# Performance work log

Measured on AMD Instinct MI355X. Metric: run time of the kernel, lower is better.

## Reference

```python
import jax, jax.numpy as jnp
import numpy as np

SQRT2 = 1.4142135623730951
MH_C = 0.8673250705840776  # (2/sqrt(3)) * pi**(-1/4), mexican-hat normalizer


def _bn(x, eps=1e-5):
    # BatchNorm (training-mode batch stats, default affine gamma=1, beta=0)
    mu = jnp.mean(x, axis=0, keepdims=True)
    var = jnp.var(x, axis=0, keepdims=True)
    return (x - mu) / jnp.sqrt(var + eps)


def setup_inputs() -> dict:
    key = jax.random.key(0)
    ks = jax.random.split(key, 10)
    N, F, E, B, OUT = 1024, 1024, 32768, 16, 10
    H = F // 2  # 512 after Haar DWT
    x = jax.random.normal(ks[0], (N, F), dtype=jnp.float32)
    edge_index = jax.random.randint(ks[1], (2, E), 0, N, dtype=jnp.int32)
    batch = jnp.sort(jax.random.randint(ks[2], (N,), 0, B, dtype=jnp.int32))
    w_att = jax.random.normal(ks[3], (2,), dtype=jnp.float32)  # Linear(2,1,bias=False)
    wk_scale = jnp.ones((H, H), dtype=jnp.float32)
    wk_trans = jax.random.normal(ks[4], (H, H), dtype=jnp.float32) * 0.1
    wk_wav_w = jax.random.normal(ks[5], (H, H), dtype=jnp.float32) * 0.05
    wk_base_w = jax.random.normal(ks[6], (H, H), dtype=jnp.float32) * 0.05
    fc1_w = jax.random.normal(ks[7], (512, F + H), dtype=jnp.float32) * 0.02
    fc1_b = jnp.zeros((512,), dtype=jnp.float32)
    fc2_w = jax.random.normal(ks[8], (OUT, 512), dtype=jnp.float32) * 0.02
    fc2_b = jnp.zeros((OUT,), dtype=jnp.float32)
    return {"x": x, "w_att": w_att, "wk_scale": wk_scale, "wk_trans": wk_trans,
            "wk_wav_w": wk_wav_w, "wk_base_w": wk_base_w, "fc1_w": fc1_w,
            "fc1_b": fc1_b, "fc2_w": fc2_w, "fc2_b": fc2_b,
            "edge_index": edge_index, "batch": batch, "num_graphs": B}


def reference(x, w_att, wk_scale, wk_trans, wk_wav_w, wk_base_w,
              fc1_w, fc1_b, fc2_w, fc2_b, edge_index, batch, num_graphs):
    N = x.shape[0]
    # --- WaveletAttention: Haar ('db1') DWT over the feature dim ---
    xe, xo = x[:, 0::2], x[:, 1::2]
    low = (xe + xo) / SQRT2            # [N, 512]
    high = (xe - xo) / SQRT2           # [N, 512]
    scores = jax.nn.sigmoid(low * w_att[0] + high * w_att[1])
    h = scores * low + (1.0 - scores) * high
    # --- GINConv aggregation (eps=0): self + sum of neighbor features ---
    src, dst = edge_index[0], edge_index[1]
    agg = h + jax.ops.segment_sum(h[src], dst, num_segments=N)  # [N, 512]
    # --- WavKAN layer 512->512 (mexican hat) ---
    xs = (agg[:, None, :] - wk_trans) / wk_scale                # [N, 512, 512]
    xs2 = xs * xs
    mh = MH_C * (1.0 - xs2) * jnp.exp(-0.5 * xs2)
    wav = jnp.einsum('noi,oi->no', mh, wk_wav_w)                # [N, 512]
    base = jax.nn.silu(agg) @ wk_base_w.T
    conv_out = _bn(wav + base)   # WavKAN-internal BatchNorm1d
    conv_out = _bn(conv_out)     # bn1 (dropout p=0 -> identity)
    # --- skip concat + bn2 ---
    z = _bn(jnp.concatenate([x, conv_out], axis=1))             # [N, 1536]
    # --- global mean pool over graphs ---
    sums = jax.ops.segment_sum(z, batch, num_segments=num_graphs)
    cnts = jax.ops.segment_sum(jnp.ones((N,), z.dtype), batch, num_segments=num_graphs)
    pooled = sums / jnp.maximum(cnts, 1.0)[:, None]             # [B, 1536]
    # --- classifier head (eval-mode dropout = identity) ---
    h1 = jax.nn.relu(pooled @ fc1_w.T + fc1_b)
    return h1 @ fc2_w.T + fc2_b
```

## Files before the change

### kernel.cpp

```cpp
#include <hip/hip_runtime.h>
#include <math.h>

#define N_NODES 1024
#define F_DIM   1024
#define H_DIM   512
#define E_EDGES 32768
#define B_GRAPHS 16
#define OUT_DIM 10
#define FH_DIM  1536
#define EPS 1e-5f
#define MH_C_D 0.8673250705840776
#define C2_D   0.72134752044448170368
#define C2_F   ((float)C2_D)
#define CSC    0.84932180028801904272f
#define WC2F   ((float)(MH_C_D / C2_D))
#define INV_SQRT2 0.70710678118654752440f

typedef float v2f __attribute__((ext_vector_type(2)));
typedef unsigned int u32;
typedef const __attribute__((address_space(1))) u32 gu32;
typedef __attribute__((address_space(3))) u32 lu32;

#if __has_builtin(__builtin_amdgcn_exp2f)
#define EXP2NEG(x) __builtin_amdgcn_exp2f(-(x))
#else
#define EXP2NEG(x) __expf(-0.69314718055994530942f * (x))
#endif

#define PK_FMA_BB(d, a, p) \
    asm("v_pk_fma_f32 %0, %1, %2, %2 op_sel:[0,0,1] op_sel_hi:[1,0,1]" \
        : "=v"(d) : "v"(a), "v"(p))
#define PK_MUL2(d, a, b) \
    asm("v_pk_mul_f32 %0, %1, %2" : "=v"(d) : "v"(a), "v"(b))
#define PK_WZC(d, s, k) \
    asm("v_pk_mul_f32 %0, %1, %2 op_sel:[0,0] op_sel_hi:[0,1]" \
        : "=v"(d) : "v"(s), "v"(k))
#define PK_FMA_HI_ACC(acc, s, p) \
    asm("v_pk_fma_f32 %0, %1, %2, %0 op_sel:[0,1,0] op_sel_hi:[1,1,1]" \
        : "+v"(acc) : "v"(s), "v"(p))

__global__ __launch_bounds__(256) void k_setup(const float* __restrict__ x,
                                               const float* __restrict__ watt,
                                               float* __restrict__ h,
                                               float* __restrict__ zbase) {
    const int bid = blockIdx.x;
    const int t = threadIdx.x;
    if (bid < 2048) {
        int idx = bid * 256 + t;
        float2 p = ((const float2*)x)[idx];
        float lo = (p.x + p.y) * INV_SQRT2;
        float hi = (p.x - p.y) * INV_SQRT2;
        float tt = lo * watt[0] + hi * watt[1];
        float sc = 1.0f / (1.0f + __expf(-tt));
        h[idx] = sc * lo + (1.0f - sc) * hi;
    } else {
        zbase[(bid - 2048) * 256 + t] = 0.0f;
    }
}

__global__ __launch_bounds__(256) void k_hx(const int* __restrict__ dst,
                                            int* __restrict__ deg,
                                            const float* __restrict__ x,
                                            float* __restrict__ xsum,
                                            float* __restrict__ xsum2,
                                            const float* __restrict__ scale,
                                            const float* __restrict__ trans,
                                            const float* __restrict__ ww,
                                            const float* __restrict__ bw,
                                            float* __restrict__ pk) {
    const int bid = blockIdx.x;
    const int t = threadIdx.x;
    if (bid < 128) {
        int e = bid * 256 + t;
        atomicAdd(&deg[dst[e]], 1);
    } else if (bid < 192) {
        const int n0 = (bid - 128) * 16;
        float s[4] = {}, s2[4] = {};
        for (int r = 0; r < 16; ++r) {
            #pragma unroll
            for (int ch = 0; ch < 4; ++ch) {
                float v = x[(n0 + r) * F_DIM + ch * 256 + t];
                s[ch] += v; s2[ch] += v * v;
            }
        }
        #pragma unroll
        for (int ch = 0; ch < 4; ++ch) {
            unsafeAtomicAdd(&xsum[ch * 256 + t], s[ch]);
            unsafeAtomicAdd(&xsum2[ch * 256 + t], s2[ch]);
        }
    } else {
        int g = (bid - 192) * 256 + t;
        float iv = 1.0f / scale[g];
        float4 p;
        p.x = iv * CSC;
        p.y = -(trans[g] * iv * CSC);
        p.z = -(ww[g] * WC2F);
        p.w = bw[g];
        ((float4*)pk)[g] = p;
    }
}

__global__ __launch_bounds__(1024) void k_scan(const int* __restrict__ deg,
                                               int* __restrict__ start,
                                               int* __restrict__ cursor) {
    __shared__ int wsum[16];
    int t = threadIdx.x;
    int lane = t & 63, wid = t >> 6;
    int v = deg[t];
    int x = v;
    #pragma unroll
    for (int off = 1; off < 64; off <<= 1) {
        int y = __shfl_up(x, off, 64);
        if (lane >= off) x += y;
    }
    if (lane == 63) wsum[wid] = x;
    __syncthreads();
    if (t < 16) {
        int w = wsum[t];
        int xs = w;
        #pragma unroll
        for (int off = 1; off < 16; off <<= 1) {
            int y = __shfl_up(xs, off, 64);
            if (t >= off) xs += y;
        }
        wsum[t] = xs - w;
    }
    __syncthreads();
    int excl = wsum[wid] + x - v;
    start[t] = excl;
    cursor[t] = excl;
}

__global__ __launch_bounds__(256) void k_fill(const int* __restrict__ src,
                                              const int* __restrict__ dst,
                                              int* __restrict__ cursor,
                                              int* __restrict__ elist) {
    int e = blockIdx.x * 256 + threadIdx.x;
    int slot = atomicAdd(&cursor[dst[e]], 1);
    elist[slot] = src[e];
}

__global__ __launch_bounds__(256) void k_gather(const float* __restrict__ h,
                                                const int* __restrict__ start,
                                                const int* __restrict__ deg,
                                                const int* __restrict__ elist,
                                                float* __restrict__ agg) {
    int d = blockIdx.x;
    int t = threadIdx.x;
    int st = start[d], dg = deg[d];
    const float2* h2 = (const float2*)h;
    float2 a = h2[d * 256 + t];
    int k = 0;
    for (; k + 4 <= dg; k += 4) {
        int s0 = elist[st + k];
        int s1 = elist[st + k + 1];
        int s2 = elist[st + k + 2];
        int s3 = elist[st + k + 3];
        float2 v0 = h2[s0 * 256 + t];
        float2 v1 = h2[s1 * 256 + t];
        float2 v2 = h2[s2 * 256 + t];
        float2 v3 = h2[s3 * 256 + t];
        a.x += (v0.x + v1.x) + (v2.x + v3.x);
        a.y += (v0.y + v1.y) + (v2.y + v3.y);
    }
    for (; k < dg; ++k) {
        int s0 = elist[st + k];
        float2 v0 = h2[s0 * 256 + t];
        a.x += v0.x; a.y += v0.y;
    }
    ((float2*)agg)[d * 256 + t] = a;
}

__global__ __launch_bounds__(256) void k_transpose(const float* __restrict__ agg,
                                                   float* __restrict__ aggT,
                                                   float* __restrict__ siluT) {
    __shared__ float tile[64 * 65];
    const int t = threadIdx.x;
    const int n0 = blockIdx.x * 64;
    const int i0 = blockIdx.y * 64;
    #pragma unroll
    for (int v = 0; v < 4; ++v) {
        int flat = v * 256 + t;
        int r = flat >> 4, c4 = flat & 15;
        float4 a = *(const float4*)&agg[(n0 + r) * H_DIM + i0 + c4 * 4];
        tile[(c4 * 4 + 0) * 65 + r] = a.x;
        tile[(c4 * 4 + 1) * 65 + r] = a.y;
        tile[(c4 * 4 + 2) * 65 + r] = a.z;
        tile[(c4 * 4 + 3) * 65 + r] = a.w;
    }
    __syncthreads();
    #pragma unroll
    for (int v = 0; v < 4; ++v) {
        int flat = v * 256 + t;
        int il = flat >> 4, c4 = flat & 15;
        float4 a;
        a.x = tile[il * 65 + c4 * 4 + 0];
        a.y = tile[il * 65 + c4 * 4 + 1];
        a.z = tile[il * 65 + c4 * 4 + 2];
        a.w = tile[il * 65 + c4 * 4 + 3];
        int g = (i0 + il) * N_NODES + n0 + c4 * 4;
        *(float4*)&aggT[g] = a;
        float4 s;
        s.x = a.x / (1.0f + __expf(-a.x));
        s.y = a.y / (1.0f + __expf(-a.y));
        s.z = a.z / (1.0f + __expf(-a.z));
        s.w = a.w / (1.0f + __expf(-a.w));
        *(float4*)&siluT[g] = s;
    }
}

#define TN 128
#define TO 32
#define KI 16
#define TOP (TO + 1)
#define ZSPLIT 8
#define ZLEN (H_DIM / ZSPLIT)
#define NSTG (ZLEN / KI)
__global__ __launch_bounds__(256) void k_wavelet(const float* __restrict__ aggT,
                                                 const float* __restrict__ siluT,
                                                 const float* __restrict__ pk,
                                                 float* __restrict__ vbp) {
    __shared__ float  sA[2][KI * TN];
    __shared__ float  sS[2][KI * TN];
    __shared__ float4 sP4[2][KI * TOP];

    const int t  = threadIdx.x;
    const int n0 = blockIdx.x * TN;
    const int o0 = blockIdx.y * TO;
    const int z0 = blockIdx.z * ZLEN;
    const int na = (t & 15) * 4;
    const int ol = (t >> 4) * 2;

    const int srow = t >> 5, scol = (t & 31) * 4;
    const int po  = t >> 4;
    const int pii = t & 15;
    const float4* pk4 = (const float4*)pk;

    v2f accw[2][4] = {};
    v2f accb[2][4] = {};
    v2f kC2; kC2.x = 1.0f; kC2.y = -C2_F;

    {
        int g0 = (z0 + srow) * N_NODES + n0 + scol;
        int g1 = (z0 + 8 + srow) * N_NODES + n0 + scol;
        __builtin_amdgcn_global_load_lds((gu32*)&aggT[g0],  (lu32*)&sA[0][t * 4], 16, 0, 0);
        __builtin_amdgcn_global_load_lds((gu32*)&aggT[g1],  (lu32*)&sA[0][1024 + t * 4], 16, 0, 0);
        __builtin_amdgcn_global_load_lds((gu32*)&siluT[g0], (lu32*)&sS[0][t * 4], 16, 0, 0);
        __builtin_amdgcn_global_load_lds((gu32*)&siluT[g1], (lu32*)&sS[0][1024 + t * 4], 16, 0, 0);
        float4 r0 = pk4[(size_t)(o0 + po) * H_DIM + z0 + pii];
        float4 r1 = pk4[(size_t)(o0 + po + 16) * H_DIM + z0 + pii];
        sP4[0][pii * TOP + po]      = r0;
        sP4[0][pii * TOP + po + 16] = r1;
    }
    __syncthreads();

    for (int stg = 0; stg < NSTG; ++stg) {
        const int i0 = z0 + stg * KI;
        const int nb = (stg + 1) & 1;
        float4 r0, r1;
        if (stg + 1 < NSTG) {
            int g0 = (i0 + KI + srow) * N_NODES + n0 + scol;
            int g1 = (i0 + KI + 8 + srow) * N_NODES + n0 + scol;
            __builtin_amdgcn_global_load_lds((gu32*)&aggT[g0],
                                             (lu32*)&sA[nb][t * 4], 16, 0, 0);
            __builtin_amdgcn_global_load_lds((gu32*)&aggT[g1],
                                             (lu32*)&sA[nb][1024 + t * 4], 16, 0, 0);
            __builtin_amdgcn_global_load_lds((gu32*)&siluT[g0],
                                             (lu32*)&sS[nb][t * 4], 16, 0, 0);
            __builtin_amdgcn_global_load_lds((gu32*)&siluT[g1],
                                             (lu32*)&sS[nb][1024 + t * 4], 16, 0, 0);
            r0 = pk4[(size_t)(o0 + po) * H_DIM + i0 + KI + pii];
            r1 = pk4[(size_t)(o0 + po + 16) * H_DIM + i0 + KI + pii];
        }
        const float*  pA = sA[stg & 1];
        const float*  pS = sS[stg & 1];
        const float4* pP = sP4[stg & 1];
        #pragma unroll 4
        for (int ii = 0; ii < KI; ++ii) {
            float4 af0 = *(const float4*)&pA[ii * TN + na];
            float4 af1 = *(const float4*)&pA[ii * TN + 64 + na];
            float4 sf0 = *(const float4*)&pS[ii * TN + na];
            float4 sf1 = *(const float4*)&pS[ii * TN + 64 + na];
            v2f a01 = {af0.x, af0.y}, a23 = {af0.z, af0.w};
            v2f a45 = {af1.x, af1.y}, a67 = {af1.z, af1.w};
            v2f s01 = {sf0.x, sf0.y}, s23 = {sf0.z, sf0.w};
            v2f s45 = {sf1.x, sf1.y}, s67 = {sf1.z, sf1.w};
            #pragma unroll
            for (int oo = 0; oo < 2; ++oo) {
                float4 pq = pP[ii * TOP + ol + oo];
                v2f pxy = {pq.x, pq.y};
                v2f pzw = {pq.z, pq.w};
                v2f wzc; PK_WZC(wzc, pzw, kC2);
                v2f y0, y1, y2, y3, q0, q1, q2, q3, w0, w1, w2, w3;
                PK_FMA_BB(y0, a01, pxy); PK_FMA_BB(y1, a23, pxy);
                PK_FMA_BB(y2, a45, pxy); PK_FMA_BB(y3, a67, pxy);
                PK_MUL2(q0, y0, y0); PK_MUL2(q1, y1, y1);
                PK_MUL2(q2, y2, y2); PK_MUL2(q3, y3, y3);
                PK_FMA_BB(w0, q0, wzc); PK_FMA_BB(w1, q1, wzc);
                PK_FMA_BB(w2, q2, wzc); PK_FMA_BB(w3, q3, wzc);
                accw[oo][0].x += w0.x * EXP2NEG(q0.x);
                accw[oo][0].y += w0.y * EXP2NEG(q0.y);
                accw[oo][1].x += w1.x * EXP2NEG(q1.x);
                accw[oo][1].y += w1.y * EXP2NEG(q1.y);
                accw[oo][2].x += w2.x * EXP2NEG(q2.x);
                accw[oo][2].y += w2.y * EXP2NEG(q2.y);
                accw[oo][3].x += w3.x * EXP2NEG(q3.x);
                accw[oo][3].y += w3.y * EXP2NEG(q3.y);
                PK_FMA_HI_ACC(accb[oo][0], s01, pzw);
                PK_FMA_HI_ACC(accb[oo][1], s23, pzw);
                PK_FMA_HI_ACC(accb[oo][2], s45, pzw);
                PK_FMA_HI_ACC(accb[oo][3], s67, pzw);
            }
        }
        if (stg + 1 < NSTG) {
            sP4[nb][pii * TOP + po]      = r0;
            sP4[nb][pii * TOP + po + 16] = r1;
        }
        __syncthreads();
    }
    float* out = vbp + (size_t)blockIdx.z * (N_NODES * H_DIM);
    #pragma unroll
    for (int p = 0; p < 4; ++p) {
        int rn = n0 + ((p & 2) ? 64 : 0) + na + (p & 1) * 2;
        float2 lo, hi;
        lo.x = accw[0][p].x + accb[0][p].x;
        lo.y = accw[1][p].x + accb[1][p].x;
        hi.x = accw[0][p].y + accb[0][p].y;
        hi.y = accw[1][p].y + accb[1][p].y;
        *(float2*)&out[(size_t)rn * H_DIM + o0 + ol]       = lo;
        *(float2*)&out[(size_t)(rn + 1) * H_DIM + o0 + ol] = hi;
    }
}

__global__ __launch_bounds__(256) void k_reduce(const float* __restrict__ vbp,
                                                float* __restrict__ vb,
                                                float* __restrict__ colsum,
                                                float* __restrict__ colsum2) {
    const int b = blockIdx.x;
    const int o0 = (b & 7) * 64;
    const int n0 = (b >> 3) * 64;
    const int t = threadIdx.x;
    const int oc = o0 + (t & 63);
    const int nsub = t >> 6;
    float s = 0.f, s2 = 0.f;
    for (int r = 0; r < 16; ++r) {
        int n = n0 + r * 4 + nsub;
        size_t idx = (size_t)n * H_DIM + oc;
        float v = 0.f;
        #pragma unroll
        for (int z = 0; z < ZSPLIT; ++z) v += vbp[z * (N_NODES * H_DIM) + idx];
        vb[idx] = v;
        s += v; s2 += v * v;
    }
    __shared__ float sh1[256], sh2[256];
    sh1[t] = s; sh2[t] = s2;
    __syncthreads();
    if (t < 64) {
        s  = sh1[t] + sh1[t + 64] + sh1[t + 128] + sh1[t + 192];
        s2 = sh2[t] + sh2[t + 64] + sh2[t + 128] + sh2[t + 192];
        unsafeAtomicAdd(&colsum[o0 + t], s);
        unsafeAtomicAdd(&colsum2[o0 + t], s2);
    }
}

__global__ __launch_bounds__(256) void k_pool(const float* __restrict__ x,
                                              const float* __restrict__ vb,
                                              const int* __restrict__ batch,
                                              const float* __restrict__ colsum,
                                              const float* __restrict__ colsum2,
                                              const float* __restrict__ xsum,
                                              const float* __restrict__ xsum2,
                                              float* __restrict__ pooled) {
    const int b = blockIdx.x;
    const int ch = blockIdx.y;
    const int t = threadIdx.x;

    __shared__ int s_cnt[4];
    __shared__ int s_st;
    int c = 0;
    for (int n = t; n < N_NODES; n += 256) {
        int bb = batch[n];
        int pb = (n == 0) ? -1 : batch[n - 1];
        c += (bb == b) ? 1 : 0;
        if (bb == b && pb != b) s_st = n;
    }
    #pragma unroll
    for (int off = 32; off > 0; off >>= 1) c += __shfl_down(c, off);
    if ((t & 63) == 0) s_cnt[t >> 6] = c;
    __syncthreads();
    int cnt = s_cnt[0] + s_cnt[1] + s_cnt[2] + s_cnt[3];
    int st = (cnt > 0) ? s_st : 0;
    float ic = (cnt > 0) ? 1.0f / (float)cnt : 0.f;

    float acc = 0.f;
    if (ch < 4) {
        int col = ch * 256 + t;
        float mu  = xsum[col] * (1.0f / N_NODES);
        float var = xsum2[col] * (1.0f / N_NODES) - mu * mu;
        if (var < 0.f) var = 0.f;
        float S = 1.0f / sqrtf(var + EPS);
        const float* base = x + col;
        for (int r = 0; r < cnt; ++r) acc += base[(size_t)(st + r) * F_DIM];
        pooled[b * FH_DIM + col] = (acc * ic - mu) * S;
    } else {
        int col = (ch - 4) * 256 + t;
        float mu  = colsum[col] * (1.0f / N_NODES);
        float var = colsum2[col] * (1.0f / N_NODES) - mu * mu;
        if (var < 0.f) var = 0.f;
        float s1v = 1.0f / sqrtf(var + EPS);
        float v1  = var * s1v * s1v;
        float s2v = 1.0f / sqrtf(v1 + EPS);
        float v2  = v1 * s2v * s2v;
        float s3v = 1.0f / sqrtf(v2 + EPS);
        float S = s1v * s2v * s3v;
        const float* base = vb + col;
        for (int r = 0; r < cnt; ++r) acc += base[(size_t)(st + r) * H_DIM];
        pooled[b * FH_DIM + F_DIM + col] = (acc * ic - mu) * S;
    }
}

__global__ __launch_bounds__(256) void k_fc1(const float* __restrict__ pooled,
                                             const float* __restrict__ w,
                                             const float* __restrict__ bias,
                                             float* __restrict__ h1) {
    int wid = (blockIdx.x * 256 + threadIdx.x) >> 6;
    int lane = threadIdx.x & 63;
    int b = wid >> 9, o = wid & 511;
    const float4* pr = (const float4*)(pooled + b * FH_DIM);
    const float4* wr = (const float4*)(w + o * FH_DIM);
    float acc = 0.f;
    #pragma unroll
    for (int k = 0; k < 6; ++k) {
        float4 a = pr[k * 64 + lane];
        float4 v = wr[k * 64 + lane];
        acc += a.x * v.x + a.y * v.y + a.z * v.z + a.w * v.w;
    }
    #pragma unroll
    for (int off = 32; off > 0; off >>= 1) acc += __shfl_down(acc, off);
    if (lane == 0) h1[b * H_DIM + o] = fmaxf(acc + bias[o], 0.f);
}

__global__ __launch_bounds__(256) void k_fc2(const float* __restrict__ h1,
                                             const float* __restrict__ w,
                                             const float* __restrict__ bias,
                                             float* __restrict__ outp) {
    int wid = (blockIdx.x * 256 + threadIdx.x) >> 6;
    int lane = threadIdx.x & 63;
    if (wid >= B_GRAPHS * OUT_DIM) return;
    int b = wid / OUT_DIM, u = wid % OUT_DIM;
    const float4* hr = (const float4*)(h1 + b * H_DIM);
    const float4* wr = (const float4*)(w + u * H_DIM);
    float acc = 0.f;
    #pragma unroll
    for (int k = 0; k < 2; ++k) {
        float4 a = hr[k * 64 + lane];
        float4 v = wr[k * 64 + lane];
        acc += a.x * v.x + a.y * v.y + a.z * v.z + a.w * v.w;
    }
    #pragma unroll
    for (int off = 32; off > 0; off >>= 1) acc += __shfl_down(acc, off);
    if (lane == 0) outp[b * OUT_DIM + u] = acc + bias[u];
}

extern "C" void kernel_launch(void* const* d_in, const int* in_sizes, int n_in,
                              void* d_out, int out_size, void* d_ws, size_t ws_size,
                              hipStream_t stream) {
    const float* x       = (const float*)d_in[0];
    const float* w_att   = (const float*)d_in[1];
    const float* wk_scale= (const float*)d_in[2];
    const float* wk_trans= (const float*)d_in[3];
    const float* wk_wav  = (const float*)d_in[4];
    const float* wk_base = (const float*)d_in[5];
    const float* fc1_w   = (const float*)d_in[6];
    const float* fc1_b   = (const float*)d_in[7];
    const float* fc2_w   = (const float*)d_in[8];
    const float* fc2_b   = (const float*)d_in[9];
    const int*   eidx    = (const int*)d_in[10];
    const int*   batch   = (const int*)d_in[11];
    float* outp = (float*)d_out;

    float* ws = (float*)d_ws;
    const int NH = N_NODES * H_DIM;
    float* h      = ws;
    float* agg    = h + NH;
    float* aggT   = agg + NH;
    float* siluT  = aggT + NH;
    float* pk     = siluT + NH;
    float* vbp    = pk + 4 * (H_DIM * H_DIM);
    float* vb     = vbp + (size_t)ZSPLIT * NH;
    float* colsum = vb + NH;
    float* colsum2= colsum + 512;
    float* xsum   = colsum2 + 512;
    float* xsum2  = xsum + 1024;
    int*   deg    = (int*)(xsum2 + 1024);
    int*   estart = deg + N_NODES;
    int*   cursor = estart + N_NODES;
    int*   elist  = cursor + N_NODES;
    float* pooled = (float*)(elist + E_EDGES);
    float* h1     = pooled + B_GRAPHS * FH_DIM;

    const int* src = eidx;
    const int* dst = eidx + E_EDGES;

    k_setup<<<2064, 256, 0, stream>>>(x, w_att, h, colsum);
    k_hx<<<1216, 256, 0, stream>>>(dst, deg, x, xsum, xsum2,
                                   wk_scale, wk_trans, wk_wav, wk_base, pk);
    k_scan<<<1, N_NODES, 0, stream>>>(deg, estart, cursor);
    k_fill<<<E_EDGES / 256, 256, 0, stream>>>(src, dst, cursor, elist);
    k_gather<<<N_NODES, 256, 0, stream>>>(h, estart, deg, elist, agg);
    {
        dim3 grid(N_NODES / 64, H_DIM / 64);
        k_transpose<<<grid, 256, 0, stream>>>(agg, aggT, siluT);
    }
    {
        dim3 grid(N_NODES / TN, H_DIM / TO, ZSPLIT);
        k_wavelet<<<grid, 256, 0, stream>>>(aggT, siluT, pk, vbp);
    }
    k_reduce<<<128, 256, 0, stream>>>(vbp, vb, colsum, colsum2);
    {
        dim3 grid(B_GRAPHS, 6);
        k_pool<<<grid, 256, 0, stream>>>(x, vb, batch, colsum, colsum2, xsum, xsum2, pooled);
    }
    k_fc1<<<(B_GRAPHS * H_DIM * 64) / 256, 256, 0, stream>>>(pooled, fc1_w, fc1_b, h1);
    k_fc2<<<(B_GRAPHS * OUT_DIM * 64 + 255) / 256, 256, 0, stream>>>(h1, fc2_w, fc2_b, outp);
}
```

Baseline: 197.6 us.

## Merge setup into k_hx and fuse pool, fc1, fc2 into one head kernel

Folds the Haar/attention setup work into the existing multi-role k_hx launch and replaces the zeroing blocks with a hipMemsetAsync covering the colsum/xsum accumulators. It also fuses mean pooling, fc1 and fc2 into a single k_head kernel with one 1024-thread block per graph, keeping pooled and h1 in shared memory. The aim is to remove several launch gaps and global round-trips of intermediate buffers. The cost is that the head now runs on only 16 blocks, and each block rereads the whole fc1 weight matrix with far less parallelism.

```diff
diff --git a/kernel.cpp b/kernel.cpp
--- a/kernel.cpp
+++ b/kernel.cpp
@@ -39,10 +39,18 @@
     asm("v_pk_fma_f32 %0, %1, %2, %0 op_sel:[0,1,0] op_sel_hi:[1,1,1]" \
         : "+v"(acc) : "v"(s), "v"(p))
 
-__global__ __launch_bounds__(256) void k_setup(const float* __restrict__ x,
-                                               const float* __restrict__ watt,
-                                               float* __restrict__ h,
-                                               float* __restrict__ zbase) {
+__global__ __launch_bounds__(256) void k_hx(const int* __restrict__ dst,
+                                            int* __restrict__ deg,
+                                            const float* __restrict__ x,
+                                            float* __restrict__ xsum,
+                                            float* __restrict__ xsum2,
+                                            const float* __restrict__ scale,
+                                            const float* __restrict__ trans,
+                                            const float* __restrict__ ww,
+                                            const float* __restrict__ bw,
+                                            float* __restrict__ pk,
+                                            const float* __restrict__ watt,
+                                            float* __restrict__ h) {
     const int bid = blockIdx.x;
     const int t = threadIdx.x;
     if (bid < 2048) {
@@ -53,28 +61,20 @@
         float tt = lo * watt[0] + hi * watt[1];
         float sc = 1.0f / (1.0f + __expf(-tt));
         h[idx] = sc * lo + (1.0f - sc) * hi;
+    } else if (bid < 3072) {
+        int g = (bid - 2048) * 256 + t;
+        float iv = 1.0f / scale[g];
+        float4 p;
+        p.x = iv * CSC;
+        p.y = -(trans[g] * iv * CSC);
+        p.z = -(ww[g] * WC2F);
+        p.w = bw[g];
+        ((float4*)pk)[g] = p;
+    } else if (bid < 3200) {
+        int e = (bid - 3072) * 256 + t;
+        atomicAdd(&deg[dst[e]], 1);
     } else {
-        zbase[(bid - 2048) * 256 + t] = 0.0f;
-    }
-}
-
-__global__ __launch_bounds__(256) void k_hx(const int* __restrict__ dst,
-                                            int* __restrict__ deg,
-                                            const float* __restrict__ x,
-                                            float* __restrict__ xsum,
-                                            float* __restrict__ xsum2,
-                                            const float* __restrict__ scale,
-                                            const float* __restrict__ trans,
-                                            const float* __restrict__ ww,
-                                            const float* __restrict__ bw,
-                                            float* __restrict__ pk) {
-    const int bid = blockIdx.x;
-    const int t = threadIdx.x;
-    if (bid < 128) {
-        int e = bid * 256 + t;
-        atomicAdd(&deg[dst[e]], 1);
-    } else if (bid < 192) {
-        const int n0 = (bid - 128) * 16;
+        const int n0 = (bid - 3200) * 16;
         float s[4] = {}, s2[4] = {};
         for (int r = 0; r < 16; ++r) {
             #pragma unroll
@@ -88,15 +88,6 @@
             unsafeAtomicAdd(&xsum[ch * 256 + t], s[ch]);
             unsafeAtomicAdd(&xsum2[ch * 256 + t], s2[ch]);
         }
-    } else {
-        int g = (bid - 192) * 256 + t;
-        float iv = 1.0f / scale[g];
-        float4 p;
-        p.x = iv * CSC;
-        p.y = -(trans[g] * iv * CSC);
-        p.z = -(ww[g] * WC2F);
-        p.w = bw[g];
-        ((float4*)pk)[g] = p;
     }
 }
 
@@ -363,47 +354,55 @@
     }
 }
 
-__global__ __launch_bounds__(256) void k_pool(const float* __restrict__ x,
-                                              const float* __restrict__ vb,
-                                              const int* __restrict__ batch,
-                                              const float* __restrict__ colsum,
-                                              const float* __restrict__ colsum2,
-                                              const float* __restrict__ xsum,
-                                              const float* __restrict__ xsum2,
-                                              float* __restrict__ pooled) {
+__global__ __launch_bounds__(1024) void k_head(const float* __restrict__ x,
+                                               const float* __restrict__ vb,
+                                               const int* __restrict__ batch,
+                                               const float* __restrict__ colsum,
+                                               const float* __restrict__ colsum2,
+                                               const float* __restrict__ xsum,
+                                               const float* __restrict__ xsum2,
+                                               const float* __restrict__ fc1w,
+                                               const float* __restrict__ fc1b,
+                                               const float* __restrict__ fc2w,
+                                               const float* __restrict__ fc2b,
+                                               float* __restrict__ outp) {
+    __shared__ __align__(16) float sp[FH_DIM];
+    __shared__ __align__(16) float sh1v[H_DIM];
+    __shared__ int s_cnt[16];
+    __shared__ int s_st;
     const int b = blockIdx.x;
-    const int ch = blockIdx.y;
     const int t = threadIdx.x;
-
-    __shared__ int s_cnt[4];
-    __shared__ int s_st;
-    int c = 0;
-    for (int n = t; n < N_NODES; n += 256) {
-        int bb = batch[n];
-        int pb = (n == 0) ? -1 : batch[n - 1];
-        c += (bb == b) ? 1 : 0;
-        if (bb == b && pb != b) s_st = n;
-    }
+    const int lane = t & 63, wv = t >> 6;
+
+    {
+        int bb = batch[t];
+        int pb = (t == 0) ? -1 : batch[t - 1];
+        int c = (bb == b) ? 1 : 0;
+        if (bb == b && pb != b) s_st = t;
+        #pragma unroll
+        for (int off = 32; off > 0; off >>= 1) c += __shfl_down(c, off);
+        if (lane == 0) s_cnt[wv] = c;
+    }
+    __syncthreads();
+    int cnt = 0;
     #pragma unroll
-    for (int off = 32; off > 0; off >>= 1) c += __shfl_down(c, off);
-    if ((t & 63) == 0) s_cnt[t >> 6] = c;
-    __syncthreads();
-    int cnt = s_cnt[0] + s_cnt[1] + s_cnt[2] + s_cnt[3];
+    for (int q = 0; q < 16; ++q) cnt += s_cnt[q];
     int st = (cnt > 0) ? s_st : 0;
     float ic = (cnt > 0) ? 1.0f / (float)cnt : 0.f;
 
-    float acc = 0.f;
-    if (ch < 4) {
-        int col = ch * 256 + t;
+    {
+        int col = t;
         float mu  = xsum[col] * (1.0f / N_NODES);
         float var = xsum2[col] * (1.0f / N_NODES) - mu * mu;
         if (var < 0.f) var = 0.f;
         float S = 1.0f / sqrtf(var + EPS);
+        float acc = 0.f;
         const float* base = x + col;
         for (int r = 0; r < cnt; ++r) acc += base[(size_t)(st + r) * F_DIM];
-        pooled[b * FH_DIM + col] = (acc * ic - mu) * S;
-    } else {
-        int col = (ch - 4) * 256 + t;
+        sp[col] = (acc * ic - mu) * S;
+    }
+    if (t < H_DIM) {
+        int col = t;
         float mu  = colsum[col] * (1.0f / N_NODES);
         float var = colsum2[col] * (1.0f / N_NODES) - mu * mu;
         if (var < 0.f) var = 0.f;
@@ -413,53 +412,46 @@
         float v2  = v1 * s2v * s2v;
         float s3v = 1.0f / sqrtf(v2 + EPS);
         float S = s1v * s2v * s3v;
+        float acc = 0.f;
         const float* base = vb + col;
         for (int r = 0; r < cnt; ++r) acc += base[(size_t)(st + r) * H_DIM];
-        pooled[b * FH_DIM + F_DIM + col] = (acc * ic - mu) * S;
-    }
-}
-
-__global__ __launch_bounds__(256) void k_fc1(const float* __restrict__ pooled,
-                                             const float* __restrict__ w,
-                                             const float* __restrict__ bias,
-                                             float* __restrict__ h1) {
-    int wid = (blockIdx.x * 256 + threadIdx.x) >> 6;
-    int lane = threadIdx.x & 63;
-    int b = wid >> 9, o = wid & 511;
-    const float4* pr = (const float4*)(pooled + b * FH_DIM);
-    const float4* wr = (const float4*)(w + o * FH_DIM);
-    float acc = 0.f;
-    #pragma unroll
-    for (int k = 0; k < 6; ++k) {
-        float4 a = pr[k * 64 + lane];
-        float4 v = wr[k * 64 + lane];
-        acc += a.x * v.x + a.y * v.y + a.z * v.z + a.w * v.w;
-    }
-    #pragma unroll
-    for (int off = 32; off > 0; off >>= 1) acc += __shfl_down(acc, off);
-    if (lane == 0) h1[b * H_DIM + o] = fmaxf(acc + bias[o], 0.f);
-}
-
-__global__ __launch_bounds__(256) void k_fc2(const float* __restrict__ h1,
-                                             const float* __restrict__ w,
-                                             const float* __restrict__ bias,
-                                             float* __restrict__ outp) {
-    int wid = (blockIdx.x * 256 + threadIdx.x) >> 6;
-    int lane = threadIdx.x & 63;
-    if (wid >= B_GRAPHS * OUT_DIM) return;
-    int b = wid / OUT_DIM, u = wid % OUT_DIM;
-    const float4* hr = (const float4*)(h1 + b * H_DIM);
-    const float4* wr = (const float4*)(w + u * H_DIM);
-    float acc = 0.f;
-    #pragma unroll
-    for (int k = 0; k < 2; ++k) {
-        float4 a = hr[k * 64 + lane];
-        float4 v = wr[k * 64 + lane];
-        acc += a.x * v.x + a.y * v.y + a.z * v.z + a.w * v.w;
-    }
-    #pragma unroll
-    for (int off = 32; off > 0; off >>= 1) acc += __shfl_down(acc, off);
-    if (lane == 0) outp[b * OUT_DIM + u] = acc + bias[u];
+        sp[F_DIM + col] = (acc * ic - mu) * S;
+    }
+    __syncthreads();
+
+    {
+        const float4* pr = (const float4*)sp;
+        for (int oi = 0; oi < 32; ++oi) {
+            int o = wv * 32 + oi;
+            const float4* wr = (const float4*)(fc1w + o * FH_DIM);
+            float acc = 0.f;
+            #pragma unroll
+            for (int k = 0; k < 6; ++k) {
+                float4 aa = pr[k * 64 + lane];
+                float4 vv = wr[k * 64 + lane];
+                acc += aa.x * vv.x + aa.y * vv.y + aa.z * vv.z + aa.w * vv.w;
+            }
+            #pragma unroll
+            for (int off = 32; off > 0; off >>= 1) acc += __shfl_down(acc, off);
+            if (lane == 0) sh1v[o] = fmaxf(acc + fc1b[o], 0.f);
+        }
+    }
+    __syncthreads();
+
+    if (wv < OUT_DIM) {
+        const float4* hr = (const float4*)sh1v;
+        const float4* wr = (const float4*)(fc2w + wv * H_DIM);
+        float acc = 0.f;
+        #pragma unroll
+        for (int k = 0; k < 2; ++k) {
+            float4 aa = hr[k * 64 + lane];
+            float4 vv = wr[k * 64 + lane];
+            acc += aa.x * vv.x + aa.y * vv.y + aa.z * vv.z + aa.w * vv.w;
+        }
+        #pragma unroll
+        for (int off = 32; off > 0; off >>= 1) acc += __shfl_down(acc, off);
+        if (lane == 0) outp[b * OUT_DIM + wv] = acc + fc2b[wv];
+    }
 }
 
 extern "C" void kernel_launch(void* const* d_in, const int* in_sizes, int n_in,
@@ -496,15 +488,13 @@
     int*   estart = deg + N_NODES;
     int*   cursor = estart + N_NODES;
     int*   elist  = cursor + N_NODES;
-    float* pooled = (float*)(elist + E_EDGES);
-    float* h1     = pooled + B_GRAPHS * FH_DIM;
 
     const int* src = eidx;
     const int* dst = eidx + E_EDGES;
 
-    k_setup<<<2064, 256, 0, stream>>>(x, w_att, h, colsum);
-    k_hx<<<1216, 256, 0, stream>>>(dst, deg, x, xsum, xsum2,
-                                   wk_scale, wk_trans, wk_wav, wk_base, pk);
+    hipMemsetAsync(colsum, 0, 4096 * sizeof(float), stream);
+    k_hx<<<3264, 256, 0, stream>>>(dst, deg, x, xsum, xsum2,
+                                   wk_scale, wk_trans, wk_wav, wk_base, pk, w_att, h);
     k_scan<<<1, N_NODES, 0, stream>>>(deg, estart, cursor);
     k_fill<<<E_EDGES / 256, 256, 0, stream>>>(src, dst, cursor, elist);
     k_gather<<<N_NODES, 256, 0, stream>>>(h, estart, deg, elist, agg);
@@ -517,10 +507,6 @@
         k_wavelet<<<grid, 256, 0, stream>>>(aggT, siluT, pk, vbp);
     }
     k_reduce<<<128, 256, 0, stream>>>(vbp, vb, colsum, colsum2);
-    {
-        dim3 grid(B_GRAPHS, 6);
-        k_pool<<<grid, 256, 0, stream>>>(x, vb, batch, colsum, colsum2, xsum, xsum2, pooled);
-    }
-    k_fc1<<<(B_GRAPHS * H_DIM * 64) / 256, 256, 0, stream>>>(pooled, fc1_w, fc1_b, h1);
-    k_fc2<<<(B_GRAPHS * OUT_DIM * 64 + 255) / 256, 256, 0, stream>>>(h1, fc2_w, fc2_b, outp);
-}
+    k_head<<<B_GRAPHS, 1024, 0, stream>>>(x, vb, batch, colsum, colsum2, xsum, xsum2,
+                                          fc1_w, fc1_b, fc2_w, fc2_b, outp);
+}
```

Result: slower. 237.1 us (+20.0%).

## Replace CSR scan/fill with fixed-capacity per-node edge buckets and merge setup kernels

Applied to the files above, without the earlier changes.

Builds the adjacency list in one pass by atomically claiming slots in a fixed 128-entry bucket per destination node, which removes the degree count, prefix scan and fill kernels. The setup, parameter packing, bucket fill and column statistics work now run in a single launch, and zeroing is done with a memset. This cuts several kernel launches and serial dependencies ahead of the gather. In exchange it assumes no node receives more than 128 edges; a node that does would overflow its bucket. It also relies on the memset clearing deg and xsum, which lie in the memset range.

```diff
diff --git a/kernel.cpp b/kernel.cpp
--- a/kernel.cpp
+++ b/kernel.cpp
@@ -15,6 +15,7 @@
 #define CSC    0.84932180028801904272f
 #define WC2F   ((float)(MH_C_D / C2_D))
 #define INV_SQRT2 0.70710678118654752440f
+#define ECAP 128
 
 typedef float v2f __attribute__((ext_vector_type(2)));
 typedef unsigned int u32;
@@ -39,10 +40,20 @@
     asm("v_pk_fma_f32 %0, %1, %2, %0 op_sel:[0,1,0] op_sel_hi:[1,1,1]" \
         : "+v"(acc) : "v"(s), "v"(p))
 
-__global__ __launch_bounds__(256) void k_setup(const float* __restrict__ x,
-                                               const float* __restrict__ watt,
-                                               float* __restrict__ h,
-                                               float* __restrict__ zbase) {
+__global__ __launch_bounds__(256) void k_hx(const int* __restrict__ src,
+                                            const int* __restrict__ dst,
+                                            int* __restrict__ deg,
+                                            int* __restrict__ elist,
+                                            const float* __restrict__ x,
+                                            float* __restrict__ xsum,
+                                            float* __restrict__ xsum2,
+                                            const float* __restrict__ scale,
+                                            const float* __restrict__ trans,
+                                            const float* __restrict__ ww,
+                                            const float* __restrict__ bw,
+                                            float* __restrict__ pk,
+                                            const float* __restrict__ watt,
+                                            float* __restrict__ h) {
     const int bid = blockIdx.x;
     const int t = threadIdx.x;
     if (bid < 2048) {
@@ -53,28 +64,22 @@
         float tt = lo * watt[0] + hi * watt[1];
         float sc = 1.0f / (1.0f + __expf(-tt));
         h[idx] = sc * lo + (1.0f - sc) * hi;
+    } else if (bid < 3072) {
+        int g = (bid - 2048) * 256 + t;
+        float iv = 1.0f / scale[g];
+        float4 p;
+        p.x = iv * CSC;
+        p.y = -(trans[g] * iv * CSC);
+        p.z = -(ww[g] * WC2F);
+        p.w = bw[g];
+        ((float4*)pk)[g] = p;
+    } else if (bid < 3200) {
+        int e = (bid - 3072) * 256 + t;
+        int d = dst[e];
+        int slot = atomicAdd(&deg[d], 1);
+        elist[d * ECAP + slot] = src[e];
     } else {
-        zbase[(bid - 2048) * 256 + t] = 0.0f;
-    }
-}
-
-__global__ __launch_bounds__(256) void k_hx(const int* __restrict__ dst,
-                                            int* __restrict__ deg,
-                                            const float* __restrict__ x,
-                                            float* __restrict__ xsum,
-                                            float* __restrict__ xsum2,
-                                            const float* __restrict__ scale,
-                                            const float* __restrict__ trans,
-                                            const float* __restrict__ ww,
-                                            const float* __restrict__ bw,
-                                            float* __restrict__ pk) {
-    const int bid = blockIdx.x;
-    const int t = threadIdx.x;
-    if (bid < 128) {
-        int e = bid * 256 + t;
-        atomicAdd(&deg[dst[e]], 1);
-    } else if (bid < 192) {
-        const int n0 = (bid - 128) * 16;
+        const int n0 = (bid - 3200) * 16;
         float s[4] = {}, s2[4] = {};
         for (int r = 0; r < 16; ++r) {
             #pragma unroll
@@ -88,66 +93,16 @@
             unsafeAtomicAdd(&xsum[ch * 256 + t], s[ch]);
             unsafeAtomicAdd(&xsum2[ch * 256 + t], s2[ch]);
         }
-    } else {
-        int g = (bid - 192) * 256 + t;
-        float iv = 1.0f / scale[g];
-        float4 p;
-        p.x = iv * CSC;
-        p.y = -(trans[g] * iv * CSC);
-        p.z = -(ww[g] * WC2F);
-        p.w = bw[g];
-        ((float4*)pk)[g] = p;
-    }
-}
-
-__global__ __launch_bounds__(1024) void k_scan(const int* __restrict__ deg,
-                                               int* __restrict__ start,
-                                               int* __restrict__ cursor) {
-    __shared__ int wsum[16];
-    int t = threadIdx.x;
-    int lane = t & 63, wid = t >> 6;
-    int v = deg[t];
-    int x = v;
-    #pragma unroll
-    for (int off = 1; off < 64; off <<= 1) {
-        int y = __shfl_up(x, off, 64);
-        if (lane >= off) x += y;
-    }
-    if (lane == 63) wsum[wid] = x;
-    __syncthreads();
-    if (t < 16) {
-        int w = wsum[t];
-        int xs = w;
-        #pragma unroll
-        for (int off = 1; off < 16; off <<= 1) {
-            int y = __shfl_up(xs, off, 64);
-            if (t >= off) xs += y;
-        }
-        wsum[t] = xs - w;
-    }
-    __syncthreads();
-    int excl = wsum[wid] + x - v;
-    start[t] = excl;
-    cursor[t] = excl;
-}
-
-__global__ __launch_bounds__(256) void k_fill(const int* __restrict__ src,
-                                              const int* __restrict__ dst,
-                                              int* __restrict__ cursor,
-                                              int* __restrict__ elist) {
-    int e = blockIdx.x * 256 + threadIdx.x;
-    int slot = atomicAdd(&cursor[dst[e]], 1);
-    elist[slot] = src[e];
+    }
 }
 
 __global__ __launch_bounds__(256) void k_gather(const float* __restrict__ h,
-                                                const int* __restrict__ start,
                                                 const int* __restrict__ deg,
                                                 const int* __restrict__ elist,
                                                 float* __restrict__ agg) {
     int d = blockIdx.x;
     int t = threadIdx.x;
-    int st = start[d], dg = deg[d];
+    int st = d * ECAP, dg = deg[d];
     const float2* h2 = (const float2*)h;
     float2 a = h2[d * 256 + t];
     int k = 0;
@@ -493,21 +448,17 @@
     float* xsum   = colsum2 + 512;
     float* xsum2  = xsum + 1024;
     int*   deg    = (int*)(xsum2 + 1024);
-    int*   estart = deg + N_NODES;
-    int*   cursor = estart + N_NODES;
-    int*   elist  = cursor + N_NODES;
-    float* pooled = (float*)(elist + E_EDGES);
+    int*   elist  = deg + N_NODES;
+    float* pooled = (float*)(elist + N_NODES * ECAP);
     float* h1     = pooled + B_GRAPHS * FH_DIM;
 
     const int* src = eidx;
     const int* dst = eidx + E_EDGES;
 
-    k_setup<<<2064, 256, 0, stream>>>(x, w_att, h, colsum);
-    k_hx<<<1216, 256, 0, stream>>>(dst, deg, x, xsum, xsum2,
-                                   wk_scale, wk_trans, wk_wav, wk_base, pk);
-    k_scan<<<1, N_NODES, 0, stream>>>(deg, estart, cursor);
-    k_fill<<<E_EDGES / 256, 256, 0, stream>>>(src, dst, cursor, elist);
-    k_gather<<<N_NODES, 256, 0, stream>>>(h, estart, deg, elist, agg);
+    hipMemsetAsync(colsum, 0, 4096 * sizeof(float), stream);
+    k_hx<<<3264, 256, 0, stream>>>(src, dst, deg, elist, x, xsum, xsum2,
+                                   wk_scale, wk_trans, wk_wav, wk_base, pk, w_att, h);
+    k_gather<<<N_NODES, 256, 0, stream>>>(h, deg, elist, agg);
     {
         dim3 grid(N_NODES / 64, H_DIM / 64);
         k_transpose<<<grid, 256, 0, stream>>>(agg, aggT, siluT);
```

After: 185.4 us (median of 2 runs). 1.07x faster.
